# Optimization experiments

Hardware: AMD Instinct MI355X
Metric: run time of the kernel (lower is better)

## Reference

```python
import jax, jax.numpy as jnp
import numpy as np

B, S, H = 4, 1024, 1024
NH, HD = 16, 64  # num heads, head dim


def setup_inputs() -> dict:
    key = jax.random.key(0)
    ks = jax.random.split(key, 7)
    scale = 1.0 / np.sqrt(H)
    return {
        "hidden_states": jax.random.normal(ks[0], (B, S, H), jnp.float32),
        "attention_mask": jnp.zeros((B, 1, 1, S), jnp.float32),
        "Wq": jax.random.normal(ks[1], (H, H), jnp.float32) * scale,
        "bq": jnp.zeros((H,), jnp.float32),
        "Wk": jax.random.normal(ks[2], (H, H), jnp.float32) * scale,
        "bk": jnp.zeros((H,), jnp.float32),
        "Wv": jax.random.normal(ks[3], (H, H), jnp.float32) * scale,
        "bv": jnp.zeros((H,), jnp.float32),
    }


def _heads(x):
    # [B,S,H] -> [B,NH,S,HD]
    return x.reshape(x.shape[0], x.shape[1], NH, HD).transpose(0, 2, 1, 3)


def reference(hidden_states, attention_mask, Wq, bq, Wk, bk, Wv, bv):
    q = _heads(hidden_states @ Wq + bq)  # [B,NH,S,HD]
    k = _heads(hidden_states @ Wk + bk)
    v = _heads(hidden_states @ Wv + bv)
    scores = jnp.einsum("bhqd,bhkd->bhqk", q, k) / np.sqrt(HD)
    scores = scores + attention_mask  # broadcast additive mask
    probs = jax.nn.softmax(scores, axis=-1)  # dropout p=0 (eval)
    ctx = jnp.einsum("bhqk,bhkd->bhqd", probs, v)
    # [B,NH,S,HD] -> [B,S,H]
    return ctx.transpose(0, 2, 1, 3).reshape(hidden_states.shape[0], hidden_states.shape[1], NH * HD)
```

## Files before the change

### kernel.cpp

```cpp
#include <hip/hip_runtime.h>
#include <hip/hip_bf16.h>

typedef __bf16 bf16_t;
typedef __bf16 bf16x8 __attribute__((ext_vector_type(8)));
typedef float f32x4 __attribute__((ext_vector_type(4)));
typedef float f32x16 __attribute__((ext_vector_type(16)));
typedef unsigned uint2v __attribute__((ext_vector_type(2)));

#define MFMA16(a, b, c) __builtin_amdgcn_mfma_f32_16x16x32_bf16((a), (b), (c), 0, 0, 0)
#define MFMA32(a, b, c) __builtin_amdgcn_mfma_f32_32x32x16_bf16((a), (b), (c), 0, 0, 0)

static constexpr int BB = 4, SS = 1024, HH = 1024, NHEAD = 16, HDIM = 64;
static constexpr int MM = BB * SS;

__device__ __forceinline__ void gload_lds16(const void* g, void* l) {
  __builtin_amdgcn_global_load_lds((const __attribute__((address_space(1))) void*)g,
                                   (__attribute__((address_space(3))) void*)l, 16, 0, 0);
}

#if __has_builtin(__builtin_amdgcn_permlane32_swap)
#define PSWAP(a, b)                                                    \
  {                                                                    \
    uint2v _r = __builtin_amdgcn_permlane32_swap((a), (b), false, false); \
    (a) = _r.x;                                                        \
    (b) = _r.y;                                                        \
  }
#else
#define PSWAP(a, b) asm("v_permlane32_swap_b32 %0, %1" : "+v"(a), "+v"(b))
#endif

__device__ __forceinline__ float EXP2(float x) {
  float r;
  asm("v_exp_f32 %0, %1" : "=v"(r) : "v"(x));
  return r;
}

__global__ __launch_bounds__(256) void cvt_bf16_kernel(const float* __restrict__ in,
                                                       bf16_t* __restrict__ out, int n) {
  int i = (blockIdx.x * 256 + threadIdx.x) * 8;
  if (i >= n) return;
  float4 a = *(const float4*)(in + i);
  float4 b = *(const float4*)(in + i + 4);
  union { int4 i4; bf16_t h[8]; } u;
  u.h[0] = (bf16_t)a.x; u.h[1] = (bf16_t)a.y; u.h[2] = (bf16_t)a.z; u.h[3] = (bf16_t)a.w;
  u.h[4] = (bf16_t)b.x; u.h[5] = (bf16_t)b.y; u.h[6] = (bf16_t)b.z; u.h[7] = (bf16_t)b.w;
  *(int4*)(out + i) = u.i4;
}

__global__ __launch_bounds__(256) void transposeW_kernel(const float* __restrict__ Wq,
                                                         const float* __restrict__ Wk,
                                                         const float* __restrict__ Wv,
                                                         bf16_t* __restrict__ WT) {
  __shared__ float tile[32][33];
  int z = blockIdx.z;
  const float* W = (z == 0) ? Wq : (z == 1) ? Wk : Wv;
  bf16_t* Out = WT + (size_t)z * HH * HH;
  int tx = threadIdx.x, ty = threadIdx.y;
  int x0 = blockIdx.x * 32;
  int y0 = blockIdx.y * 32;
  for (int j = ty; j < 32; j += 8)
    tile[j][tx] = W[(size_t)(y0 + j) * HH + x0 + tx];
  __syncthreads();
  for (int j = ty; j < 32; j += 8)
    Out[(size_t)(x0 + j) * HH + y0 + tx] = (bf16_t)tile[tx][j];
}

#define BMT 128
#define BNT 384
#define BKT 64
#define NTL 16
#define BUFBYTES 65536

__global__ __launch_bounds__(512, 2) void qkv_gemm2(const bf16_t* __restrict__ hiddenB,
                                                    const bf16_t* __restrict__ WT,
                                                    const float* __restrict__ bq,
                                                    const float* __restrict__ bk,
                                                    const float* __restrict__ bv,
                                                    bf16_t* __restrict__ Qo,
                                                    bf16_t* __restrict__ Ko,
                                                    bf16_t* __restrict__ Vt) {
  __shared__ bf16_t smem[2 * BUFBYTES / 2];

  const int wg = blockIdx.x;
  const int id = (wg & 7) * 32 + (wg >> 3);
  const int nb = id & 7;
  const int mb = id >> 3;

  const int t = threadIdx.x;
  const int lane = t & 63;
  const int w = t >> 6;
  const int wr = w >> 2;
  const int wc = w & 3;
  const int lr = lane & 15;
  const int g4 = lane >> 4;

  const unsigned schunk = (((unsigned)(t & 7)) ^ ((unsigned)((t >> 3) & 7))) << 4;
  const char* Ag = (const char*)hiddenB + (size_t)(mb * BMT) * 2048;
  const char* Bg = (const char*)WT + (size_t)(nb * BNT) * 2048;

  auto stage = [&](const char* gb, int growbase, int kbyte, char* ldsdest) {
    gload_lds16(gb + (size_t)(growbase + (t >> 3)) * 2048 + kbyte + schunk,
                ldsdest + w * 1024);
  };
  const unsigned axor = ((unsigned)(lr & 7)) << 4;

  f32x4 acc[4][6] = {};

  {
    char* S0 = (char*)smem;
    stage(Ag, 0, 0, S0);
    stage(Ag, 64, 0, S0 + 8192);
#pragma unroll
    for (int i = 0; i < 6; ++i) stage(Bg, i * 64, 0, S0 + 16384 + i * 8192);
  }
  asm volatile("s_waitcnt vmcnt(0)" ::: "memory");
  __builtin_amdgcn_s_barrier();

  for (int j = 0; j < NTL; ++j) {
    const char* Ab = (const char*)smem + (j & 1) * BUFBYTES;
    const char* Bb = Ab + 16384;
    char* Sb = (char*)smem + ((j + 1) & 1) * BUFBYTES;
    const int kb = (j + 1) * 128;
    const bool st = (j + 1 < NTL);

    if (st) { stage(Ag, 0, kb, Sb); stage(Ag, 64, kb, Sb + 8192); }

    bf16x8 af[4][2];
#pragma unroll
    for (int mi = 0; mi < 4; ++mi)
#pragma unroll
      for (int ks = 0; ks < 2; ++ks)
        af[mi][ks] = *(const bf16x8*)(Ab + (size_t)(wr * 64 + mi * 16 + lr) * 128 +
                                      (((unsigned)(ks * 64 + g4 * 16)) ^ axor));

#pragma unroll
    for (int p = 0; p < 3; ++p) {
      if (st) {
        stage(Bg, (2 * p) * 64, kb, Sb + 16384 + (2 * p) * 8192);
        stage(Bg, (2 * p + 1) * 64, kb, Sb + 16384 + (2 * p + 1) * 8192);
      }
      bf16x8 b0[2], b1[2];
#pragma unroll
      for (int ks = 0; ks < 2; ++ks) {
        b0[ks] = *(const bf16x8*)(Bb + (size_t)(wc * 96 + (2 * p) * 16 + lr) * 128 +
                                  (((unsigned)(ks * 64 + g4 * 16)) ^ axor));
        b1[ks] = *(const bf16x8*)(Bb + (size_t)(wc * 96 + (2 * p + 1) * 16 + lr) * 128 +
                                  (((unsigned)(ks * 64 + g4 * 16)) ^ axor));
      }
      __builtin_amdgcn_s_setprio(1);
#pragma unroll
      for (int mi = 0; mi < 4; ++mi)
#pragma unroll
        for (int ks = 0; ks < 2; ++ks) {
          acc[mi][2 * p] = MFMA16(af[mi][ks], b0[ks], acc[mi][2 * p]);
          acc[mi][2 * p + 1] = MFMA16(af[mi][ks], b1[ks], acc[mi][2 * p + 1]);
        }
      __builtin_amdgcn_s_setprio(0);
    }

    if (st) {
      asm volatile("s_waitcnt vmcnt(0)" ::: "memory");
      __builtin_amdgcn_s_barrier();
    }
  }

#pragma unroll
  for (int ni = 0; ni < 6; ++ni) {
    int col = nb * BNT + wc * 96 + ni * 16 + lr;
    int z = col >> 10;
    int ci = col & 1023;
    const float* bias = (z == 0) ? bq : (z == 1) ? bk : bv;
    float bia = bias[ci];
    int hh = ci >> 6, d = ci & 63;
    if (z < 2) {
      bf16_t* Out = (z == 0) ? Qo : Ko;
#pragma unroll
      for (int mi = 0; mi < 4; ++mi) {
#pragma unroll
        for (int r = 0; r < 4; ++r) {
          int row = mb * BMT + wr * 64 + mi * 16 + g4 * 4 + r;
          int b = row >> 10, s = row & 1023;
          Out[((size_t)(b * NHEAD + hh) * SS + s) * HDIM + d] = (bf16_t)(acc[mi][ni][r] + bia);
        }
      }
    } else {
#pragma unroll
      for (int mi = 0; mi < 4; ++mi) {
        int row0 = mb * BMT + wr * 64 + mi * 16 + g4 * 4;
        int b = row0 >> 10, s0 = row0 & 1023;
        float v0 = acc[mi][ni][0] + bia, v1 = acc[mi][ni][1] + bia;
        float v2 = acc[mi][ni][2] + bia, v3 = acc[mi][ni][3] + bia;
        unsigned u0, u1;
        asm("v_cvt_pk_bf16_f32 %0, %1, %2" : "=v"(u0) : "v"(v0), "v"(v1));
        asm("v_cvt_pk_bf16_f32 %0, %1, %2" : "=v"(u1) : "v"(v2), "v"(v3));
        uint2 pv; pv.x = u0; pv.y = u1;
        *(uint2*)&Vt[((size_t)(b * NHEAD + hh) * HDIM + d) * SS + s0] = pv;
      }
    }
  }
}

__global__ __launch_bounds__(512, 4) void attn6_kernel(const bf16_t* __restrict__ Q,
                                                       const bf16_t* __restrict__ K,
                                                       const bf16_t* __restrict__ Vt,
                                                       const float* __restrict__ mask,
                                                       float* __restrict__ out) {
  __shared__ bf16_t KVsm[2][2][2][64 * 64];
  __shared__ float Msm[SS];

  const int wg = blockIdx.x;
  const int id = (wg & 7) * 64 + (wg >> 3);
  const int xblk = id & 7;
  const int bh = id >> 3;

  const int b = bh >> 4;
  const int h = bh & 15;
  const int t = threadIdx.x;
  const int lane = t & 63;
  const int w = t >> 6;
  const int wl = w & 3;
  const int half = w >> 2;
  const int l31 = lane & 31;
  const int hi = lane >> 5;
  const int q0 = xblk * 128 + wl * 32;
  const int kvbase = half * 512;

  const bf16_t* Qh = Q + (size_t)bh * SS * HDIM;
  const bf16_t* Kh = K + (size_t)bh * SS * HDIM;
  const bf16_t* Vh = Vt + (size_t)bh * HDIM * SS;

  const float L2E = 1.4426950408889634f;
  if (t < 256) {
    float4 mv = *(const float4*)&mask[(size_t)b * SS + t * 4];
    mv.x *= L2E; mv.y *= L2E; mv.z *= L2E; mv.w *= L2E;
    *(float4*)&Msm[t * 4] = mv;
  }

  bf16x8 qb[4];
#pragma unroll
  for (int c = 0; c < 4; ++c) {
    bf16x8 q = *(const bf16x8*)&Qh[(size_t)(q0 + l31) * HDIM + c * 16 + hi * 8];
#pragma unroll
    for (int e = 0; e < 8; ++e) q[e] = (bf16_t)((float)q[e] * (0.125f * L2E));
    qb[c] = q;
  }

  const int srow = lane >> 3;
  const unsigned gcol = ((lane & 7) * 16) ^ (srow << 4);
  const unsigned swz = (unsigned)((l31 & 7) << 4);

  auto stageKV = [&](int tile, int buf) {
    const int kv0 = kvbase + tile * 64;
#pragma unroll
    for (int i = 0; i < 2; ++i) {
      int rbase = wl * 16 + i * 8;
      gload_lds16((const char*)Kh + (size_t)(kv0 + rbase + srow) * 128 + gcol,
                  (char*)&KVsm[half][buf][0][0] + (size_t)rbase * 128);
      gload_lds16((const char*)Vh + (size_t)(rbase + srow) * 2048 + (size_t)kv0 * 2 + gcol,
                  (char*)&KVsm[half][buf][1][0] + (size_t)rbase * 128);
    }
  };

  f32x16 acc0 = {}, acc1 = {};
  float m_run = -1e30f, l_run = 0.f;

  stageKV(0, 0);
  asm volatile("s_waitcnt vmcnt(0)" ::: "memory");
  __builtin_amdgcn_s_barrier();

  for (int tt = 0; tt < 8; ++tt) {
    if (tt + 1 < 8) stageKV(tt + 1, (tt + 1) & 1);
    const char* Kb = (const char*)&KVsm[half][tt & 1][0][0];
    const char* Vb = (const char*)&KVsm[half][tt & 1][1][0];
    const int kv0 = kvbase + tt * 64;

    f32x16 st0 = {}, st1 = {};
    __builtin_amdgcn_s_setprio(1);
#pragma unroll
    for (int c = 0; c < 4; ++c) {
      bf16x8 kf0 = *(const bf16x8*)(Kb + (size_t)l31 * 128 + ((unsigned)(c * 32 + hi * 16) ^ swz));
      st0 = MFMA32(kf0, qb[c], st0);
    }
#pragma unroll
    for (int c = 0; c < 4; ++c) {
      bf16x8 kf1 = *(const bf16x8*)(Kb + (size_t)(32 + l31) * 128 + ((unsigned)(c * 32 + hi * 16) ^ swz));
      st1 = MFMA32(kf1, qb[c], st1);
    }
    __builtin_amdgcn_s_setprio(0);

#pragma unroll
    for (int k2 = 0; k2 < 8; ++k2) {
      int off = 8 * (k2 >> 1) + 4 * hi + 2 * (k2 & 1);
      float2 m0v = *(const float2*)&Msm[kv0 + off];
      float2 m1v = *(const float2*)&Msm[kv0 + 32 + off];
      st0[2 * k2] += m0v.x; st0[2 * k2 + 1] += m0v.y;
      st1[2 * k2] += m1v.x; st1[2 * k2 + 1] += m1v.y;
    }

    float v0 = fmaxf(st0[0], st1[0]),  v1 = fmaxf(st0[1], st1[1]);
    float v2 = fmaxf(st0[2], st1[2]),  v3 = fmaxf(st0[3], st1[3]);
    float v4 = fmaxf(st0[4], st1[4]),  v5 = fmaxf(st0[5], st1[5]);
    float v6 = fmaxf(st0[6], st1[6]),  v7 = fmaxf(st0[7], st1[7]);
    float v8 = fmaxf(st0[8], st1[8]),  v9 = fmaxf(st0[9], st1[9]);
    float v10 = fmaxf(st0[10], st1[10]), v11 = fmaxf(st0[11], st1[11]);
    float v12 = fmaxf(st0[12], st1[12]), v13 = fmaxf(st0[13], st1[13]);
    float v14 = fmaxf(st0[14], st1[14]), v15 = fmaxf(st0[15], st1[15]);
    float g0 = fmaxf(fmaxf(v0, v1), v2);
    float g1 = fmaxf(fmaxf(v3, v4), v5);
    float g2 = fmaxf(fmaxf(v6, v7), v8);
    float g3 = fmaxf(fmaxf(v9, v10), v11);
    float g4 = fmaxf(fmaxf(v12, v13), v14);
    float mj = fmaxf(fmaxf(fmaxf(g0, g1), g2), fmaxf(fmaxf(g3, g4), v15));
    mj = fmaxf(mj, __shfl_xor(mj, 32));

    if (!__all(mj <= m_run + 8.f)) {
      float mnew = fmaxf(m_run, mj);
      float corr = EXP2(m_run - mnew);
#pragma unroll
      for (int r = 0; r < 16; ++r) { acc0[r] *= corr; acc1[r] *= corr; }
      l_run *= corr;
      m_run = mnew;
    }

#pragma unroll
    for (int r = 0; r < 16; ++r) st0[r] = EXP2(st0[r] - m_run);
#pragma unroll
    for (int r = 0; r < 16; ++r) st1[r] = EXP2(st1[r] - m_run);

    float s0 = (st0[0] + st1[0]) + (st0[1] + st1[1]);
    float s1 = (st0[2] + st1[2]) + (st0[3] + st1[3]);
    float s2 = (st0[4] + st1[4]) + (st0[5] + st1[5]);
    float s3 = (st0[6] + st1[6]) + (st0[7] + st1[7]);
    float s4 = (st0[8] + st1[8]) + (st0[9] + st1[9]);
    float s5 = (st0[10] + st1[10]) + (st0[11] + st1[11]);
    float s6 = (st0[12] + st1[12]) + (st0[13] + st1[13]);
    float s7 = (st0[14] + st1[14]) + (st0[15] + st1[15]);
    float ls = ((s0 + s1) + (s2 + s3)) + ((s4 + s5) + (s6 + s7));
    ls += __shfl_xor(ls, 32);
    l_run += ls;

    unsigned wd0[8], wd1[8];
#pragma unroll
    for (int k2 = 0; k2 < 8; ++k2) {
      unsigned r0, r1;
      float a0f = st0[2 * k2], a1f = st0[2 * k2 + 1];
      float b0f = st1[2 * k2], b1f = st1[2 * k2 + 1];
      asm("v_cvt_pk_bf16_f32 %0, %1, %2" : "=v"(r0) : "v"(a0f), "v"(a1f));
      asm("v_cvt_pk_bf16_f32 %0, %1, %2" : "=v"(r1) : "v"(b0f), "v"(b1f));
      wd0[k2] = r0; wd1[k2] = r1;
    }
    unsigned a0 = wd0[0], b0 = wd0[2]; PSWAP(a0, b0);
    unsigned a1 = wd0[1], b1 = wd0[3]; PSWAP(a1, b1);
    unsigned a2 = wd0[4], b2 = wd0[6]; PSWAP(a2, b2);
    unsigned a3 = wd0[5], b3 = wd0[7]; PSWAP(a3, b3);
    unsigned c0 = wd1[0], d0 = wd1[2]; PSWAP(c0, d0);
    unsigned c1 = wd1[1], d1 = wd1[3]; PSWAP(c1, d1);
    unsigned c2 = wd1[4], d2 = wd1[6]; PSWAP(c2, d2);
    unsigned c3 = wd1[5], d3 = wd1[7]; PSWAP(c3, d3);
    union { unsigned u[4]; bf16x8 v; } pf0, pf1, pf2, pf3;
    pf0.u[0] = a0; pf0.u[1] = a1; pf0.u[2] = b0; pf0.u[3] = b1;
    pf1.u[0] = a2; pf1.u[1] = a3; pf1.u[2] = b2; pf1.u[3] = b3;
    pf2.u[0] = c0; pf2.u[1] = c1; pf2.u[2] = d0; pf2.u[3] = d1;
    pf3.u[0] = c2; pf3.u[1] = c3; pf3.u[2] = d2; pf3.u[3] = d3;

    __builtin_amdgcn_s_setprio(1);
    {
      bf16x8 vf;
      vf = *(const bf16x8*)(Vb + (size_t)(l31) * 128 + ((unsigned)(0 * 32 + hi * 16) ^ swz));
      acc0 = MFMA32(vf, pf0.v, acc0);
      vf = *(const bf16x8*)(Vb + (size_t)(32 + l31) * 128 + ((unsigned)(0 * 32 + hi * 16) ^ swz));
      acc1 = MFMA32(vf, pf0.v, acc1);
      vf = *(const bf16x8*)(Vb + (size_t)(l31) * 128 + ((unsigned)(1 * 32 + hi * 16) ^ swz));
      acc0 = MFMA32(vf, pf1.v, acc0);
      vf = *(const bf16x8*)(Vb + (size_t)(32 + l31) * 128 + ((unsigned)(1 * 32 + hi * 16) ^ swz));
      acc1 = MFMA32(vf, pf1.v, acc1);
      vf = *(const bf16x8*)(Vb + (size_t)(l31) * 128 + ((unsigned)(2 * 32 + hi * 16) ^ swz));
      acc0 = MFMA32(vf, pf2.v, acc0);
      vf = *(const bf16x8*)(Vb + (size_t)(32 + l31) * 128 + ((unsigned)(2 * 32 + hi * 16) ^ swz));
      acc1 = MFMA32(vf, pf2.v, acc1);
      vf = *(const bf16x8*)(Vb + (size_t)(l31) * 128 + ((unsigned)(3 * 32 + hi * 16) ^ swz));
      acc0 = MFMA32(vf, pf3.v, acc0);
      vf = *(const bf16x8*)(Vb + (size_t)(32 + l31) * 128 + ((unsigned)(3 * 32 + hi * 16) ^ swz));
      acc1 = MFMA32(vf, pf3.v, acc1);
    }
    __builtin_amdgcn_s_setprio(0);

    asm volatile("s_waitcnt vmcnt(0)" ::: "memory");
    __builtin_amdgcn_s_barrier();
  }

  __syncthreads();
  float* mb = (float*)&KVsm[0][0][0][0];
  if (half == 1) {
    float* dst = mb + ((size_t)(wl * 64 + lane)) * 36;
#pragma unroll
    for (int g = 0; g < 4; ++g) {
      float4 w0, w1;
      w0.x = acc0[g * 4 + 0]; w0.y = acc0[g * 4 + 1];
      w0.z = acc0[g * 4 + 2]; w0.w = acc0[g * 4 + 3];
      w1.x = acc1[g * 4 + 0]; w1.y = acc1[g * 4 + 1];
      w1.z = acc1[g * 4 + 2]; w1.w = acc1[g * 4 + 3];
      *(float4*)(dst + g * 4) = w0;
      *(float4*)(dst + 16 + g * 4) = w1;
    }
    dst[32] = m_run; dst[33] = l_run;
  }
  __syncthreads();
  if (half == 0) {
    const float* src = mb + ((size_t)(wl * 64 + lane)) * 36;
    float m1 = src[32], l1 = src[33];
    float m = fmaxf(m_run, m1);
    float f0 = EXP2(m_run - m), f1 = EXP2(m1 - m);
    float rinv = 1.0f / (l_run * f0 + l1 * f1);
    float fr0 = f0 * rinv, fr1 = f1 * rinv;
    int q = q0 + l31;
    float* ob = out + ((size_t)(b * SS + q)) * HH + h * HDIM;
#pragma unroll
    for (int g = 0; g < 4; ++g) {
      float4 o0, o1;
      o0.x = acc0[g * 4 + 0] * fr0 + src[g * 4 + 0] * fr1;
      o0.y = acc0[g * 4 + 1] * fr0 + src[g * 4 + 1] * fr1;
      o0.z = acc0[g * 4 + 2] * fr0 + src[g * 4 + 2] * fr1;
      o0.w = acc0[g * 4 + 3] * fr0 + src[g * 4 + 3] * fr1;
      o1.x = acc1[g * 4 + 0] * fr0 + src[16 + g * 4 + 0] * fr1;
      o1.y = acc1[g * 4 + 1] * fr0 + src[16 + g * 4 + 1] * fr1;
      o1.z = acc1[g * 4 + 2] * fr0 + src[16 + g * 4 + 2] * fr1;
      o1.w = acc1[g * 4 + 3] * fr0 + src[16 + g * 4 + 3] * fr1;
      *(float4*)&ob[g * 8 + 4 * hi] = o0;
      *(float4*)&ob[32 + g * 8 + 4 * hi] = o1;
    }
  }
}

extern "C" void kernel_launch(void* const* d_in, const int* in_sizes, int n_in,
                              void* d_out, int out_size, void* d_ws, size_t ws_size,
                              hipStream_t stream) {
  const float* hs   = (const float*)d_in[0];
  const float* mask = (const float*)d_in[1];
  const float* Wq   = (const float*)d_in[2];
  const float* bq   = (const float*)d_in[3];
  const float* Wk   = (const float*)d_in[4];
  const float* bk   = (const float*)d_in[5];
  const float* Wv   = (const float*)d_in[6];
  const float* bv   = (const float*)d_in[7];
  float* out = (float*)d_out;

  char* ws = (char*)d_ws;
  bf16_t* hiddenB = (bf16_t*)ws;
  bf16_t* WT      = (bf16_t*)(ws + (size_t)8 * 1024 * 1024);
  bf16_t* Qb      = (bf16_t*)(ws + (size_t)14 * 1024 * 1024);
  bf16_t* Kb      = (bf16_t*)(ws + (size_t)22 * 1024 * 1024);
  bf16_t* Vt      = (bf16_t*)(ws + (size_t)30 * 1024 * 1024);

  cvt_bf16_kernel<<<MM * HH / (256 * 8), 256, 0, stream>>>(hs, hiddenB, MM * HH);
  transposeW_kernel<<<dim3(32, 32, 3), dim3(32, 8), 0, stream>>>(Wq, Wk, Wv, WT);
  qkv_gemm2<<<256, 512, 0, stream>>>(hiddenB, WT, bq, bk, bv, Qb, Kb, Vt);
  attn6_kernel<<<512, 512, 0, stream>>>(Qb, Kb, Vt, mask, out);
}
```

Before: 75.00 us.

## Software-pipeline attention loop: overlap QK^T of tile t with PV of tile t-1

Restructures the attention main loop so each iteration computes QK^T for the current KV tile and then runs the PV MFMAs for the previous tile's packed probabilities, with the softmax/pack step deferred to the end of the iteration. The intent is to interleave independent MFMA work with the exp/max/convert VALU work and hide latency between softmax and PV. It adds a prologue and epilogue, keeps packed P in registers across iterations (more register pressure), and adds an extra barrier before staging the next tile into the buffer that the PV step just read.

```diff
diff --git a/kernel.cpp b/kernel.cpp
--- a/kernel.cpp
+++ b/kernel.cpp
@@ -200,7 +200,7 @@
   }
 }
 
-__global__ __launch_bounds__(512, 4) void attn6_kernel(const bf16_t* __restrict__ Q,
+__global__ __launch_bounds__(512, 4) void attn7_kernel(const bf16_t* __restrict__ Q,
                                                        const bf16_t* __restrict__ K,
                                                        const bf16_t* __restrict__ Vt,
                                                        const float* __restrict__ mask,
@@ -263,18 +263,9 @@
 
   f32x16 acc0 = {}, acc1 = {};
   float m_run = -1e30f, l_run = 0.f;
-
-  stageKV(0, 0);
-  asm volatile("s_waitcnt vmcnt(0)" ::: "memory");
-  __builtin_amdgcn_s_barrier();
-
-  for (int tt = 0; tt < 8; ++tt) {
-    if (tt + 1 < 8) stageKV(tt + 1, (tt + 1) & 1);
-    const char* Kb = (const char*)&KVsm[half][tt & 1][0][0];
-    const char* Vb = (const char*)&KVsm[half][tt & 1][1][0];
-    const int kv0 = kvbase + tt * 64;
-
-    f32x16 st0 = {}, st1 = {};
+  unsigned pfp[16];
+
+  auto qkt = [&](const char* Kb, f32x16& st0, f32x16& st1) {
     __builtin_amdgcn_s_setprio(1);
 #pragma unroll
     for (int c = 0; c < 4; ++c) {
@@ -287,7 +278,36 @@
       st1 = MFMA32(kf1, qb[c], st1);
     }
     __builtin_amdgcn_s_setprio(0);
-
+  };
+
+  auto pv = [&](const char* Vb) {
+    union { unsigned u[4]; bf16x8 v; } pf0, pf1, pf2, pf3;
+    pf0.u[0] = pfp[0]; pf0.u[1] = pfp[1]; pf0.u[2] = pfp[2]; pf0.u[3] = pfp[3];
+    pf1.u[0] = pfp[4]; pf1.u[1] = pfp[5]; pf1.u[2] = pfp[6]; pf1.u[3] = pfp[7];
+    pf2.u[0] = pfp[8]; pf2.u[1] = pfp[9]; pf2.u[2] = pfp[10]; pf2.u[3] = pfp[11];
+    pf3.u[0] = pfp[12]; pf3.u[1] = pfp[13]; pf3.u[2] = pfp[14]; pf3.u[3] = pfp[15];
+    __builtin_amdgcn_s_setprio(1);
+    bf16x8 vf;
+    vf = *(const bf16x8*)(Vb + (size_t)(l31) * 128 + ((unsigned)(0 * 32 + hi * 16) ^ swz));
+    acc0 = MFMA32(vf, pf0.v, acc0);
+    vf = *(const bf16x8*)(Vb + (size_t)(32 + l31) * 128 + ((unsigned)(0 * 32 + hi * 16) ^ swz));
+    acc1 = MFMA32(vf, pf0.v, acc1);
+    vf = *(const bf16x8*)(Vb + (size_t)(l31) * 128 + ((unsigned)(1 * 32 + hi * 16) ^ swz));
+    acc0 = MFMA32(vf, pf1.v, acc0);
+    vf = *(const bf16x8*)(Vb + (size_t)(32 + l31) * 128 + ((unsigned)(1 * 32 + hi * 16) ^ swz));
+    acc1 = MFMA32(vf, pf1.v, acc1);
+    vf = *(const bf16x8*)(Vb + (size_t)(l31) * 128 + ((unsigned)(2 * 32 + hi * 16) ^ swz));
+    acc0 = MFMA32(vf, pf2.v, acc0);
+    vf = *(const bf16x8*)(Vb + (size_t)(32 + l31) * 128 + ((unsigned)(2 * 32 + hi * 16) ^ swz));
+    acc1 = MFMA32(vf, pf2.v, acc1);
+    vf = *(const bf16x8*)(Vb + (size_t)(l31) * 128 + ((unsigned)(3 * 32 + hi * 16) ^ swz));
+    acc0 = MFMA32(vf, pf3.v, acc0);
+    vf = *(const bf16x8*)(Vb + (size_t)(32 + l31) * 128 + ((unsigned)(3 * 32 + hi * 16) ^ swz));
+    acc1 = MFMA32(vf, pf3.v, acc1);
+    __builtin_amdgcn_s_setprio(0);
+  };
+
+  auto smpack = [&](int kv0, f32x16& st0, f32x16& st1) {
 #pragma unroll
     for (int k2 = 0; k2 < 8; ++k2) {
       int off = 8 * (k2 >> 1) + 4 * hi + 2 * (k2 & 1);
@@ -296,7 +316,6 @@
       st0[2 * k2] += m0v.x; st0[2 * k2 + 1] += m0v.y;
       st1[2 * k2] += m1v.x; st1[2 * k2 + 1] += m1v.y;
     }
-
     float v0 = fmaxf(st0[0], st1[0]),  v1 = fmaxf(st0[1], st1[1]);
     float v2 = fmaxf(st0[2], st1[2]),  v3 = fmaxf(st0[3], st1[3]);
     float v4 = fmaxf(st0[4], st1[4]),  v5 = fmaxf(st0[5], st1[5]);
@@ -312,7 +331,6 @@
     float g4 = fmaxf(fmaxf(v12, v13), v14);
     float mj = fmaxf(fmaxf(fmaxf(g0, g1), g2), fmaxf(fmaxf(g3, g4), v15));
     mj = fmaxf(mj, __shfl_xor(mj, 32));
-
     if (!__all(mj <= m_run + 8.f)) {
       float mnew = fmaxf(m_run, mj);
       float corr = EXP2(m_run - mnew);
@@ -321,12 +339,10 @@
       l_run *= corr;
       m_run = mnew;
     }
-
 #pragma unroll
     for (int r = 0; r < 16; ++r) st0[r] = EXP2(st0[r] - m_run);
 #pragma unroll
     for (int r = 0; r < 16; ++r) st1[r] = EXP2(st1[r] - m_run);
-
     float s0 = (st0[0] + st1[0]) + (st0[1] + st1[1]);
     float s1 = (st0[2] + st1[2]) + (st0[3] + st1[3]);
     float s2 = (st0[4] + st1[4]) + (st0[5] + st1[5]);
@@ -338,7 +354,6 @@
     float ls = ((s0 + s1) + (s2 + s3)) + ((s4 + s5) + (s6 + s7));
     ls += __shfl_xor(ls, 32);
     l_run += ls;
-
     unsigned wd0[8], wd1[8];
 #pragma unroll
     for (int k2 = 0; k2 < 8; ++k2) {
@@ -357,37 +372,33 @@
     unsigned c1 = wd1[1], d1 = wd1[3]; PSWAP(c1, d1);
     unsigned c2 = wd1[4], d2 = wd1[6]; PSWAP(c2, d2);
     unsigned c3 = wd1[5], d3 = wd1[7]; PSWAP(c3, d3);
-    union { unsigned u[4]; bf16x8 v; } pf0, pf1, pf2, pf3;
-    pf0.u[0] = a0; pf0.u[1] = a1; pf0.u[2] = b0; pf0.u[3] = b1;
-    pf1.u[0] = a2; pf1.u[1] = a3; pf1.u[2] = b2; pf1.u[3] = b3;
-    pf2.u[0] = c0; pf2.u[1] = c1; pf2.u[2] = d0; pf2.u[3] = d1;
-    pf3.u[0] = c2; pf3.u[1] = c3; pf3.u[2] = d2; pf3.u[3] = d3;
-
-    __builtin_amdgcn_s_setprio(1);
-    {
-      bf16x8 vf;
-      vf = *(const bf16x8*)(Vb + (size_t)(l31) * 128 + ((unsigned)(0 * 32 + hi * 16) ^ swz));
-      acc0 = MFMA32(vf, pf0.v, acc0);
-      vf = *(const bf16x8*)(Vb + (size_t)(32 + l31) * 128 + ((unsigned)(0 * 32 + hi * 16) ^ swz));
-      acc1 = MFMA32(vf, pf0.v, acc1);
-      vf = *(const bf16x8*)(Vb + (size_t)(l31) * 128 + ((unsigned)(1 * 32 + hi * 16) ^ swz));
-      acc0 = MFMA32(vf, pf1.v, acc0);
-      vf = *(const bf16x8*)(Vb + (size_t)(32 + l31) * 128 + ((unsigned)(1 * 32 + hi * 16) ^ swz));
-      acc1 = MFMA32(vf, pf1.v, acc1);
-      vf = *(const bf16x8*)(Vb + (size_t)(l31) * 128 + ((unsigned)(2 * 32 + hi * 16) ^ swz));
-      acc0 = MFMA32(vf, pf2.v, acc0);
-      vf = *(const bf16x8*)(Vb + (size_t)(32 + l31) * 128 + ((unsigned)(2 * 32 + hi * 16) ^ swz));
-      acc1 = MFMA32(vf, pf2.v, acc1);
-      vf = *(const bf16x8*)(Vb + (size_t)(l31) * 128 + ((unsigned)(3 * 32 + hi * 16) ^ swz));
-      acc0 = MFMA32(vf, pf3.v, acc0);
-      vf = *(const bf16x8*)(Vb + (size_t)(32 + l31) * 128 + ((unsigned)(3 * 32 + hi * 16) ^ swz));
-      acc1 = MFMA32(vf, pf3.v, acc1);
-    }
-    __builtin_amdgcn_s_setprio(0);
-
+    pfp[0] = a0; pfp[1] = a1; pfp[2] = b0; pfp[3] = b1;
+    pfp[4] = a2; pfp[5] = a3; pfp[6] = b2; pfp[7] = b3;
+    pfp[8] = c0; pfp[9] = c1; pfp[10] = d0; pfp[11] = d1;
+    pfp[12] = c2; pfp[13] = c3; pfp[14] = d2; pfp[15] = d3;
+  };
+
+  stageKV(0, 0);
+  asm volatile("s_waitcnt vmcnt(0) lgkmcnt(0)" ::: "memory");
+  __builtin_amdgcn_s_barrier();
+  {
+    f32x16 st0 = {}, st1 = {};
+    qkt((const char*)&KVsm[half][0][0][0], st0, st1);
+    stageKV(1, 1);
+    smpack(kvbase + 0, st0, st1);
+  }
+
+  for (int tt = 1; tt < 8; ++tt) {
     asm volatile("s_waitcnt vmcnt(0)" ::: "memory");
     __builtin_amdgcn_s_barrier();
-  }
+    f32x16 st0 = {}, st1 = {};
+    qkt((const char*)&KVsm[half][tt & 1][0][0], st0, st1);
+    pv((const char*)&KVsm[half][(tt - 1) & 1][1][0]);
+    __builtin_amdgcn_s_barrier();
+    if (tt < 7) stageKV(tt + 1, (tt + 1) & 1);
+    smpack(kvbase + tt * 64, st0, st1);
+  }
+  pv((const char*)&KVsm[half][1][1][0]);
 
   __syncthreads();
   float* mb = (float*)&KVsm[0][0][0][0];
@@ -455,5 +466,5 @@
   cvt_bf16_kernel<<<MM * HH / (256 * 8), 256, 0, stream>>>(hs, hiddenB, MM * HH);
   transposeW_kernel<<<dim3(32, 32, 3), dim3(32, 8), 0, stream>>>(Wq, Wk, Wv, WT);
   qkv_gemm2<<<256, 512, 0, stream>>>(hiddenB, WT, bq, bk, bv, Qb, Kb, Vt);
-  attn6_kernel<<<512, 512, 0, stream>>>(Qb, Kb, Vt, mask, out);
-}
+  attn7_kernel<<<512, 512, 0, stream>>>(Qb, Kb, Vt, mask, out);
+}
```

Result: no change. 75.29 us (+0.4%).
